# Optimization experiments

Hardware: AMD Instinct MI355X
Metric: run time of the kernel (lower is better)

The kernel has to match this reference:

```python
import jax, jax.numpy as jnp
import numpy as np

EPS = 1e-6
B, T, C = 2, 1024, 2048
H, KV, D = 32, 8, 128
E, F, TOPK = 8, 768, 2


def rmsnorm(x, w):
    xf = x.astype(jnp.float32)
    var = jnp.mean(xf * xf, axis=-1, keepdims=True)
    return w * (xf * jax.lax.rsqrt(var + EPS)).astype(x.dtype)


def rotate_half(x):
    d = x.shape[-1] // 2
    return jnp.concatenate([-x[..., d:], x[..., :d]], axis=-1)


def setup_inputs() -> dict:
    key = jax.random.key(0)
    ks = jax.random.split(key, 12)
    sc = 0.02
    x = jax.random.normal(ks[0], (B, T, C), dtype=jnp.float32)
    # RoPE tables: cos/sin of shape [B, T, D]
    inv_freq = 1.0 / (1e6 ** (np.arange(0, D, 2, dtype=np.float32) / D))
    pos = np.arange(T, dtype=np.float32)
    freqs = pos[:, None] * inv_freq[None, :]          # [T, D/2]
    emb = np.concatenate([freqs, freqs], axis=-1)     # [T, D]
    cos = jnp.broadcast_to(jnp.cos(emb)[None], (B, T, D)).astype(jnp.float32)
    sin = jnp.broadcast_to(jnp.sin(emb)[None], (B, T, D)).astype(jnp.float32)
    return {
        "x": x, "cos": cos, "sin": sin,
        "ln1_w": jnp.ones((C,), jnp.float32),
        "q_w": jax.random.normal(ks[1], (C, H * D), jnp.float32) * sc,
        "k_w": jax.random.normal(ks[2], (C, KV * D), jnp.float32) * sc,
        "v_w": jax.random.normal(ks[3], (C, KV * D), jnp.float32) * sc,
        "o_w": jax.random.normal(ks[4], (H * D, C), jnp.float32) * sc,
        "qn_w": jnp.ones((D,), jnp.float32),
        "kn_w": jnp.ones((D,), jnp.float32),
        "ln2_w": jnp.ones((C,), jnp.float32),
        "gate_w": jax.random.normal(ks[5], (C, E), jnp.float32) * sc,
        "gate_up_w": jax.random.normal(ks[6], (E, C, 2 * F), jnp.float32) * sc,
        "down_w": jax.random.normal(ks[7], (E, F, C), jnp.float32) * sc,
    }


def reference(x, cos, sin, ln1_w, q_w, k_w, v_w, o_w, qn_w, kn_w, ln2_w,
              gate_w, gate_up_w, down_w):
    b, t, c = x.shape
    # ---- attention branch ----
    h = rmsnorm(x, ln1_w)
    q = (h @ q_w).reshape(b, t, H, D)
    k = (h @ k_w).reshape(b, t, KV, D)
    v = (h @ v_w).reshape(b, t, KV, D)
    q = rmsnorm(q, qn_w)
    k = rmsnorm(k, kn_w)
    cb = cos[:, :, None, :]
    sb = sin[:, :, None, :]
    q = q * cb + rotate_half(q) * sb
    k = k * cb + rotate_half(k) * sb
    rep = H // KV
    k = jnp.repeat(k, rep, axis=2)  # [b,t,H,D]
    v = jnp.repeat(v, rep, axis=2)
    scores = jnp.einsum('bthd,bshd->bhts', q, k) / jnp.sqrt(jnp.float32(D))
    causal = jnp.tril(jnp.ones((t, t), dtype=bool))
    scores = jnp.where(causal, scores, jnp.finfo(scores.dtype).min)
    attn = jax.nn.softmax(scores, axis=-1)
    ao = jnp.einsum('bhts,bshd->bthd', attn, v).reshape(b, t, H * D) @ o_w
    x = x + ao
    # ---- MoE branch ----
    h2 = rmsnorm(x, ln2_w)
    hidden = h2.reshape(-1, c)                     # [N, C]
    logits = hidden @ gate_w                       # [N, E]
    rw = jax.nn.softmax(logits.astype(jnp.float32), axis=-1)
    tw, ti = jax.lax.top_k(rw, TOPK)
    tw = tw / (tw.sum(axis=-1, keepdims=True) + 1e-9)
    n = hidden.shape[0]
    routed = jnp.zeros_like(logits).at[jnp.arange(n)[:, None], ti].set(tw.astype(logits.dtype))
    routed = routed / (routed.sum(axis=-1, keepdims=True) + 1e-9)
    gu = jnp.einsum('th,ehq->teq', hidden, gate_up_w)   # [N, E, 2F]
    g, u = jnp.split(gu, 2, axis=-1)
    eo = jnp.einsum('teq,eqh->teh', jax.nn.silu(g) * u, down_w)  # [N, E, C]
    moe = (eo * routed[..., None]).sum(axis=1).reshape(b, t, c)
    return x + moe
```

## Files before the change

### kernel.cpp

```cpp
#include <hip/hip_runtime.h>
#include <hip/hip_bf16.h>

typedef short bf16x8 __attribute__((ext_vector_type(8)));
typedef float f32x4 __attribute__((ext_vector_type(4)));
typedef unsigned short u16;

#define NTOK 2048
#define CDIM 2048
#define TSEQ 1024
#define NH   32
#define NKV  8
#define DH   128
#define NE   8
#define FDIM 768
#define CAP  2048

#define GLOAD_LDS16(g, l) \
  __builtin_amdgcn_global_load_lds((const __attribute__((address_space(1))) void*)(g), \
                                   (__attribute__((address_space(3))) void*)(l), 16, 0, 0)

__device__ __forceinline__ u16 f2bf(float f){
  union { float f; unsigned u; } v; v.f = f;
  unsigned r = v.u + 0x7FFFu + ((v.u >> 16) & 1u);
  return (u16)(r >> 16);
}
__device__ __forceinline__ float bf2f(u16 x){
  union { unsigned u; float f; } v; v.u = ((unsigned)x) << 16; return v.f;
}

__device__ __forceinline__ f32x4 mfma_bf16(bf16x8 a, bf16x8 b, f32x4 c){
  return __builtin_amdgcn_mfma_f32_16x16x32_bf16(a, b, c, 0, 0, 0);
}

__device__ __forceinline__ int xcd_swz(int orig, int nwg){
  int xcd = orig & 7;
  int q = nwg >> 3, r = nwg & 7;
  int base = (xcd < r) ? xcd*(q+1) : r*(q+1) + (xcd-r)*q;
  return base + (orig >> 3);
}

__global__ void cast_transpose(const float* __restrict__ in, u16* __restrict__ out,
                               int R, int Cc, int rstride, int d1,
                               long long s_hi, long long s_lo)
{
  __shared__ u16 tile[64][72];
  int z = blockIdx.z;
  in  += (long long)(z / d1) * s_hi + (long long)(z % d1) * s_lo;
  out += (size_t)z * R * Cc;
  int r0 = blockIdx.y*64, c0 = blockIdx.x*64;
  int lr = threadIdx.x >> 4;
  int lc = (threadIdx.x & 15) * 4;
  #pragma unroll
  for(int i=0;i<4;i++){
    int r = lr + i*16;
    float4 v = *(const float4*)(in + (size_t)(r0 + r)*rstride + c0 + lc);
    tile[lc+0][r] = f2bf(v.x);
    tile[lc+1][r] = f2bf(v.y);
    tile[lc+2][r] = f2bf(v.z);
    tile[lc+3][r] = f2bf(v.w);
  }
  __syncthreads();
  int oc  = threadIdx.x >> 2;
  int orr = (threadIdx.x & 3) * 16;
  uint4 a  = *(const uint4*)&tile[oc][orr];
  uint4 b2 = *(const uint4*)&tile[oc][orr + 8];
  *(uint4*)(out + (size_t)(c0+oc)*R + r0 + orr)     = a;
  *(uint4*)(out + (size_t)(c0+oc)*R + r0 + orr + 8) = b2;
}

__global__ void cast_transpose_qkv(const float* __restrict__ qw, const float* __restrict__ kw,
                                   const float* __restrict__ vw, u16* __restrict__ wqkvT)
{
  __shared__ u16 tile[64][72];
  int bx = blockIdx.x;
  const float* in; u16* out; int rstride, c0;
  if(bx < 64){       in = qw; out = wqkvT;                        rstride = 4096; c0 = bx*64; }
  else if(bx < 80){  in = kw; out = wqkvT + (size_t)4096*2048;    rstride = 1024; c0 = (bx-64)*64; }
  else {             in = vw; out = wqkvT + (size_t)5120*2048;    rstride = 1024; c0 = (bx-80)*64; }
  const int R = 2048;
  int r0 = blockIdx.y*64;
  int lr = threadIdx.x >> 4;
  int lc = (threadIdx.x & 15) * 4;
  #pragma unroll
  for(int i=0;i<4;i++){
    int r = lr + i*16;
    float4 v = *(const float4*)(in + (size_t)(r0 + r)*rstride + c0 + lc);
    tile[lc+0][r] = f2bf(v.x);
    tile[lc+1][r] = f2bf(v.y);
    tile[lc+2][r] = f2bf(v.z);
    tile[lc+3][r] = f2bf(v.w);
  }
  __syncthreads();
  int oc  = threadIdx.x >> 2;
  int orr = (threadIdx.x & 3) * 16;
  uint4 a  = *(const uint4*)&tile[oc][orr];
  uint4 b2 = *(const uint4*)&tile[oc][orr + 8];
  *(uint4*)(out + (size_t)(c0+oc)*R + r0 + orr)     = a;
  *(uint4*)(out + (size_t)(c0+oc)*R + r0 + orr + 8) = b2;
}

__global__ void transpose_gate(const float* __restrict__ gw, float* __restrict__ gwT)
{
  int i = blockIdx.x*256 + threadIdx.x;
  int c = i >> 3, e = i & 7;
  gwT[(size_t)e*CDIM + c] = gw[(size_t)c*NE + e];
}

__global__ void transpose_u16(const u16* __restrict__ in, u16* __restrict__ out,
                              int R, int Cc, int rstride, int d1,
                              long long s_hi, long long s_lo)
{
  __shared__ u16 tile[32][34];
  int z = blockIdx.z;
  in += (long long)(z / d1) * s_hi + (long long)(z % d1) * s_lo;
  out += (size_t)z * R * Cc;
  int tx = threadIdx.x & 31, ty = threadIdx.x >> 5;
  int r0 = blockIdx.y * 32, c0 = blockIdx.x * 32;
  #pragma unroll
  for(int i=0;i<4;i++){
    int r = r0 + ty + i*8;
    if(r < R && c0 + tx < Cc) tile[ty + i*8][tx] = in[(size_t)r * rstride + c0 + tx];
  }
  __syncthreads();
  #pragma unroll
  for(int i=0;i<4;i++){
    int c = c0 + ty + i*8;
    if(c < Cc && r0 + tx < R) out[(size_t)c * R + r0 + tx] = tile[tx][ty + i*8];
  }
}

__global__ void rmsnorm_kernel(const float* __restrict__ x, const float* __restrict__ w,
                               u16* __restrict__ outb, float* __restrict__ outf)
{
  __shared__ float sbuf[4];
  int row = blockIdx.x;
  const float* xr = x + (size_t)row * CDIM;
  int t0 = threadIdx.x * 8;
  float4 v0 = *(const float4*)(xr + t0);
  float4 v1 = *(const float4*)(xr + t0 + 4);
  float a[8] = {v0.x,v0.y,v0.z,v0.w,v1.x,v1.y,v1.z,v1.w};
  float ss = 0.f;
  #pragma unroll
  for(int i=0;i<8;i++) ss += a[i]*a[i];
  #pragma unroll
  for(int o=32;o>0;o>>=1) ss += __shfl_xor(ss, o);
  if((threadIdx.x & 63) == 0) sbuf[threadIdx.x >> 6] = ss;
  __syncthreads();
  float tot = sbuf[0]+sbuf[1]+sbuf[2]+sbuf[3];
  float r = rsqrtf(tot * (1.0f/CDIM) + 1e-6f);
  float4 w0 = *(const float4*)(w + t0);
  float4 w1 = *(const float4*)(w + t0 + 4);
  float wv[8] = {w0.x,w0.y,w0.z,w0.w,w1.x,w1.y,w1.z,w1.w};
  #pragma unroll
  for(int i=0;i<8;i++){
    float o = a[i] * r * wv[i];
    outb[(size_t)row*CDIM + t0 + i] = f2bf(o);
    if(outf) outf[(size_t)row*CDIM + t0 + i] = o;
  }
}

__global__ __launch_bounds__(512, 1) void gemm256(const u16* __restrict__ A,
                                                  const u16* __restrict__ Bt,
                                                  u16* __restrict__ Cb,
                                                  int M, int N, int K)
{
  extern __shared__ u16 lds[];
  const int NT = K >> 6;
  int tid = threadIdx.x;
  int lane = tid & 63, g = lane >> 4, cl = lane & 15;
  int wid = tid >> 6, wr = wid >> 2, wc = wid & 3;
  int br = blockIdx.y * 256, bc = blockIdx.x * 192;
  int rowl[4], slotl[4], srcoff[4];
  #pragma unroll
  for(int l=0;l<4;l++){
    int c = l*512 + tid;
    rowl[l]  = c >> 3;
    slotl[l] = c & 7;
    srcoff[l] = (slotl[l] ^ (rowl[l] & 7)) * 8;
  }
  f32x4 acc[8][3];
  #pragma unroll
  for(int m=0;m<8;m++)
    #pragma unroll
    for(int n=0;n<3;n++) acc[m][n] = (f32x4){0.f,0.f,0.f,0.f};

  auto stage = [&](int t, int b){
    int k0 = t << 6;
    #pragma unroll
    for(int l=0;l<4;l++)
      GLOAD_LDS16(A  + (size_t)(br + rowl[l])*K + k0 + srcoff[l],
                  &lds[b*16384 + rowl[l]*64 + slotl[l]*8]);
    #pragma unroll
    for(int l=0;l<3;l++)
      GLOAD_LDS16(Bt + (size_t)(bc + rowl[l])*K + k0 + srcoff[l],
                  &lds[32768 + b*12288 + rowl[l]*64 + slotl[l]*8]);
  };

  stage(0, 0);
  for(int t=0;t<NT;t++){
    int buf = t & 1;
    if(t+1 < NT){
      stage(t+1, buf^1);
      asm volatile("s_waitcnt vmcnt(7)" ::: "memory");
    } else {
      asm volatile("s_waitcnt vmcnt(0)" ::: "memory");
    }
    asm volatile("s_barrier" ::: "memory");
    const u16* As_ = &lds[buf*16384];
    const u16* Bs_ = &lds[32768 + buf*12288];
    __builtin_amdgcn_s_setprio(1);
    #pragma unroll
    for(int kk=0;kk<2;kk++){
      bf16x8 a[8], b[3];
      #pragma unroll
      for(int m=0;m<8;m++){
        int row = wr*128 + m*16 + cl;
        int sl  = ((4*kk + g) ^ (row & 7)) * 8;
        a[m] = *(const bf16x8*)&As_[row*64 + sl];
      }
      #pragma unroll
      for(int n=0;n<3;n++){
        int row = wc*48 + n*16 + cl;
        int sl  = ((4*kk + g) ^ (row & 7)) * 8;
        b[n] = *(const bf16x8*)&Bs_[row*64 + sl];
      }
      #pragma unroll
      for(int m=0;m<8;m++)
        #pragma unroll
        for(int n=0;n<3;n++)
          acc[m][n] = mfma_bf16(a[m], b[n], acc[m][n]);
    }
    __builtin_amdgcn_s_setprio(0);
    asm volatile("s_barrier" ::: "memory");
  }
  #pragma unroll
  for(int m=0;m<8;m++)
    #pragma unroll
    for(int n=0;n<3;n++)
      #pragma unroll
      for(int j=0;j<4;j++){
        int row = br + wr*128 + m*16 + g*4 + j;
        int col = bc + wc*48 + n*16 + cl;
        Cb[(size_t)row*N + col] = f2bf(acc[m][n][j]);
      }
}

__global__ __launch_bounds__(256) void gemm_oproj_pipe(const u16* __restrict__ A,
                                                       const u16* __restrict__ Bt,
                                                       float* __restrict__ C,
                                                       const float* __restrict__ addsrc,
                                                       int M, int N, int K)
{
  extern __shared__ u16 lds[];
  int nwg = gridDim.x;
  int wgid = xcd_swz(blockIdx.x, nwg);
  int nbx = N >> 7;
  int bys = wgid / nbx, bxs = wgid % nbx;
  const int NT = K >> 6;
  int tid = threadIdx.x;
  int lane = tid&63, g = lane>>4, cl = lane&15;
  int w = tid>>6, wr = w>>1, wc = w&1;
  int br = bys*128, bc = bxs*128;
  int rowc[4], slotc[4], srcoff[4];
  #pragma unroll
  for(int l=0;l<4;l++){
    int c = l*256 + tid;
    rowc[l]  = c >> 3;
    slotc[l] = c & 7;
    srcoff[l] = (slotc[l] ^ (rowc[l] & 7)) * 8;
  }
  f32x4 acc[4][4];
  #pragma unroll
  for(int m=0;m<4;m++)
    #pragma unroll
    for(int n=0;n<4;n++) acc[m][n] = (f32x4){0.f,0.f,0.f,0.f};

  auto stage = [&](int t, int b){
    int k0 = t << 6;
    #pragma unroll
    for(int l=0;l<4;l++)
      GLOAD_LDS16(A + (size_t)(br + rowc[l])*K + k0 + srcoff[l],
                  &lds[b*8192 + rowc[l]*64 + slotc[l]*8]);
    #pragma unroll
    for(int l=0;l<4;l++)
      GLOAD_LDS16(Bt + (size_t)(bc + rowc[l])*K + k0 + srcoff[l],
                  &lds[16384 + b*8192 + rowc[l]*64 + slotc[l]*8]);
  };

  stage(0, 0);
  for(int t=0;t<NT;t++){
    int buf = t & 1;
    if(t+1 < NT){
      stage(t+1, buf^1);
      asm volatile("s_waitcnt vmcnt(8)" ::: "memory");
    } else {
      asm volatile("s_waitcnt vmcnt(0)" ::: "memory");
    }
    asm volatile("s_barrier" ::: "memory");
    const u16* As_ = &lds[buf*8192];
    const u16* Bs_ = &lds[16384 + buf*8192];
    __builtin_amdgcn_s_setprio(1);
    #pragma unroll
    for(int kk=0;kk<2;kk++){
      bf16x8 a[4], b[4];
      #pragma unroll
      for(int m=0;m<4;m++){
        int row = wr*64 + m*16 + cl;
        int sl  = ((4*kk + g) ^ (row & 7)) * 8;
        a[m] = *(const bf16x8*)&As_[row*64 + sl];
      }
      #pragma unroll
      for(int n=0;n<4;n++){
        int row = wc*64 + n*16 + cl;
        int sl  = ((4*kk + g) ^ (row & 7)) * 8;
        b[n] = *(const bf16x8*)&Bs_[row*64 + sl];
      }
      #pragma unroll
      for(int m=0;m<4;m++)
        #pragma unroll
        for(int n=0;n<4;n++)
          acc[m][n] = mfma_bf16(a[m], b[n], acc[m][n]);
    }
    __builtin_amdgcn_s_setprio(0);
    asm volatile("s_barrier" ::: "memory");
  }
  #pragma unroll
  for(int m=0;m<4;m++)
    #pragma unroll
    for(int n=0;n<4;n++)
      #pragma unroll
      for(int j=0;j<4;j++){
        int row = br + wr*64 + m*16 + g*4 + j;
        int col = bc + wc*64 + n*16 + cl;
        C[(size_t)row*N + col] = acc[m][n][j] + addsrc[(size_t)row*N + col];
      }
}

__global__ void qk_norm_rope(const u16* __restrict__ qkv, const float* __restrict__ cosb,
                             const float* __restrict__ sinb, const float* __restrict__ qnw,
                             const float* __restrict__ knw,
                             u16* __restrict__ qb, u16* __restrict__ kb)
{
  __shared__ float red[2];
  __shared__ float buf[128];
  int bt = blockIdx.x;
  int head = blockIdx.y;
  int d = threadIdx.x;
  int b = bt >> 10, t = bt & 1023;
  bool isq = head < NH;
  const u16* src = qkv + (size_t)bt*6144 + (isq ? head*DH : 4096 + (head-NH)*DH);
  float v = bf2f(src[d]);
  float ss = v*v;
  #pragma unroll
  for(int o=32;o>0;o>>=1) ss += __shfl_xor(ss, o);
  if((threadIdx.x & 63) == 0) red[threadIdx.x >> 6] = ss;
  __syncthreads();
  float tot = red[0] + red[1];
  float r = rsqrtf(tot * (1.0f/DH) + 1e-6f);
  float nv = v * r * (isq ? qnw[d] : knw[d]);
  buf[d] = nv;
  __syncthreads();
  float rot = (d < 64) ? -buf[d+64] : buf[d-64];
  float cs = cosb[(size_t)bt*DH + d], sn = sinb[(size_t)bt*DH + d];
  float ov = nv*cs + rot*sn;
  if(isq) ov *= 0.08838834764831845f;
  if(isq) qb[(((size_t)b*NH  + head)     *TSEQ + t)*DH + d] = f2bf(ov);
  else    kb[(((size_t)b*NKV + (head-NH))*TSEQ + t)*DH + d] = f2bf(ov);
}

__global__ __launch_bounds__(512) void attn_kernel(const u16* __restrict__ qb,
                                                   const u16* __restrict__ kb,
                                                   const u16* __restrict__ vt,
                                                   u16* __restrict__ aob)
{
  extern __shared__ u16 lds[];
  int tid = threadIdx.x;
  int w = tid>>6, lane = tid&63, g = lane>>4, cl = lane&15;
  int nwg = gridDim.x * gridDim.y * gridDim.z;
  int orig = (blockIdx.z * gridDim.y + blockIdx.y) * gridDim.x + blockIdx.x;
  int wgid = xcd_swz(orig, nwg);
  int bxs = wgid % gridDim.x;
  int bys = (wgid / gridDim.x) % gridDim.y;
  int bzs = wgid / (gridDim.x * gridDim.y);
  int b = bzs, kvh = bys, pr = bxs;
  int head = kvh*4 + (w>>1);
  int mh = w & 1;
  const u16* qp = qb + (((size_t)b*NH  + head)*TSEQ)*DH;
  const u16* kp = kb + (((size_t)b*NKV + kvh)*TSEQ)*DH;
  const u16* vp = vt + (((size_t)b*NKV + kvh)*DH)*TSEQ;
  u16* Psw = &lds[34816 + w*16*72];
  for(int idx = tid; idx < 2*16*64; idx += 512){
    int bufi = idx >> 10, rr = (idx >> 6) & 15, c2 = idx & 63;
    lds[16384 + bufi*9216 + (128 + rr)*64 + c2] = (rr == 0) ? (u16)0x3F80 : (u16)0;
  }
  __syncthreads();
  int kRow[2], kDst[2], kSrc[2], vRow[2], vDst[2], vSrc[2];
  #pragma unroll
  for(int it=0; it<2; it++){
    int c = tid + it*512;
    kRow[it] = c >> 4;
    int ks = c & 15;
    kDst[it] = kRow[it]*128 + ks*8;
    kSrc[it] = (ks ^ (kRow[it] & 7)) * 8;
    vRow[it] = c >> 3;
    int vs = c & 7;
    vDst[it] = vRow[it]*64 + vs*8;
    vSrc[it] = (vs ^ (vRow[it] & 7)) * 8;
  }
  int qts[2] = { pr, 31 - pr };
  for(int ti=0; ti<2; ti++){
    int qt = qts[ti];
    int q0 = qt*32;
    int qr0 = q0 + mh*16;
    const int NTk = (q0 + 95) >> 6;
    bf16x8 aq[4];
    #pragma unroll
    for(int kd=0;kd<4;kd++)
      aq[kd] = *(const bf16x8*)(qp + (size_t)(qr0 + cl)*DH + kd*32 + g*8);
    f32x4 accO[9];
    #pragma unroll
    for(int n=0;n<9;n++) accO[n] = (f32x4){0.f,0.f,0.f,0.f};
    float mr[4];
    #pragma unroll
    for(int j=0;j<4;j++) mr[j] = -1e30f;
    #pragma unroll
    for(int it=0; it<2; it++){
      GLOAD_LDS16(kp + (size_t)kRow[it]*DH + kSrc[it], &lds[kDst[it]]);
      GLOAD_LDS16(vp + (size_t)vRow[it]*TSEQ + vSrc[it], &lds[16384 + vDst[it]]);
    }
    for(int t=0; t<NTk; t++){
      int buf = t & 1;
      int kv0 = t*64;
      if(t+1 < NTk){
        int kv1 = kv0 + 64, nb = buf ^ 1;
        #pragma unroll
        for(int it=0; it<2; it++){
          GLOAD_LDS16(kp + (size_t)(kv1 + kRow[it])*DH + kSrc[it], &lds[nb*8192 + kDst[it]]);
          GLOAD_LDS16(vp + (size_t)vRow[it]*TSEQ + kv1 + vSrc[it], &lds[16384 + nb*9216 + vDst[it]]);
        }
        asm volatile("s_waitcnt vmcnt(4)" ::: "memory");
      } else {
        asm volatile("s_waitcnt vmcnt(0)" ::: "memory");
      }
      asm volatile("s_barrier" ::: "memory");
      const u16* Ksb = &lds[buf*8192];
      const u16* Vsb = &lds[16384 + buf*9216];
      f32x4 sc[4];
      #pragma unroll
      for(int n=0;n<4;n++) sc[n] = (f32x4){0.f,0.f,0.f,0.f};
      __builtin_amdgcn_s_setprio(1);
      #pragma unroll
      for(int kd=0;kd<4;kd++){
        bf16x8 bk[4];
        #pragma unroll
        for(int n=0;n<4;n++){
          int row = n*16 + cl;
          bk[n] = *(const bf16x8*)&Ksb[row*128 + (((kd*4 + g) ^ (cl & 7))*8)];
        }
        #pragma unroll
        for(int n=0;n<4;n++)
          sc[n] = mfma_bf16(aq[kd], bk[n], sc[n]);
      }
      __builtin_amdgcn_s_setprio(0);
      if(kv0 + 63 > q0){
        #pragma unroll
        for(int n=0;n<4;n++)
          #pragma unroll
          for(int j=0;j<4;j++){
            int row = qr0 + g*4 + j;
            int col = kv0 + n*16 + cl;
            if(col > row) sc[n][j] = -1e30f;
          }
      }
      float tmax[4];
      #pragma unroll
      for(int j=0;j<4;j++)
        tmax[j] = fmaxf(fmaxf(sc[0][j], sc[1][j]), fmaxf(sc[2][j], sc[3][j]));
      #pragma unroll
      for(int o=1;o<16;o<<=1)
        #pragma unroll
        for(int j=0;j<4;j++) tmax[j] = fmaxf(tmax[j], __shfl_xor(tmax[j], o));
      float grow = -1e30f;
      #pragma unroll
      for(int j=0;j<4;j++) grow = fmaxf(grow, tmax[j] - mr[j]);
      grow = fmaxf(grow, __shfl_xor(grow, 16));
      grow = fmaxf(grow, __shfl_xor(grow, 32));
      if(grow > 8.0f){
        #pragma unroll
        for(int j=0;j<4;j++){
          float mn = fmaxf(mr[j], tmax[j]);
          float f  = __expf(mr[j] - mn);
          mr[j] = mn;
          #pragma unroll
          for(int n=0;n<9;n++) accO[n][j] *= f;
        }
      }
      #pragma unroll
      for(int n=0;n<4;n++)
        #pragma unroll
        for(int j=0;j<4;j++)
          sc[n][j] = __expf(sc[n][j] - mr[j]);
      #pragma unroll
      for(int n=0;n<4;n++)
        #pragma unroll
        for(int j=0;j<4;j++)
          Psw[(g*4 + j)*72 + n*16 + cl] = f2bf(sc[n][j]);
      bf16x8 pa[2];
      #pragma unroll
      for(int s2=0;s2<2;s2++)
        pa[s2] = *(const bf16x8*)&Psw[cl*72 + s2*32 + g*8];
      __builtin_amdgcn_s_setprio(1);
      #pragma unroll
      for(int n=0;n<9;n++){
        #pragma unroll
        for(int s2=0;s2<2;s2++){
          bf16x8 bv = *(const bf16x8*)&Vsb[(n*16 + cl)*64 + (((s2*4 + g) ^ (cl & 7))*8)];
          accO[n] = mfma_bf16(pa[s2], bv, accO[n]);
        }
      }
      __builtin_amdgcn_s_setprio(0);
      asm volatile("s_barrier" ::: "memory");
    }
    float linv[4];
    #pragma unroll
    for(int j=0;j<4;j++){
      float l = __shfl(accO[8][j], lane & 48);
      linv[j] = 1.0f / l;
    }
    #pragma unroll
    for(int n=0;n<8;n++)
      #pragma unroll
      for(int j=0;j<4;j++){
        int row = qr0 + g*4 + j;
        float v = accO[n][j] * linv[j];
        aob[((size_t)b*TSEQ + row)*(NH*DH) + head*DH + n*16 + cl] = f2bf(v);
      }
  }
}

__global__ void route_kernel(const float* __restrict__ h2f, const float* __restrict__ gwT,
                             int* __restrict__ cnt, int* __restrict__ bidx,
                             float* __restrict__ bw)
{
  int lane = threadIdx.x & 63;
  int token = blockIdx.x*4 + (threadIdx.x >> 6);
  float acc[8];
  #pragma unroll
  for(int e=0;e<8;e++) acc[e]=0.f;
  for(int c0 = lane*4; c0 < CDIM; c0 += 256){
    float4 hv = *(const float4*)(h2f + (size_t)token*CDIM + c0);
    #pragma unroll
    for(int e=0;e<8;e++){
      float4 gv = *(const float4*)(gwT + (size_t)e*CDIM + c0);
      acc[e] += hv.x*gv.x + hv.y*gv.y + hv.z*gv.z + hv.w*gv.w;
    }
  }
  #pragma unroll
  for(int o=32;o>0;o>>=1)
    #pragma unroll
    for(int e=0;e<8;e++) acc[e] += __shfl_xor(acc[e], o);
  if(lane==0){
    float mx = acc[0];
    #pragma unroll
    for(int e=1;e<8;e++) mx = fmaxf(mx, acc[e]);
    float rw[8]; float s=0.f;
    #pragma unroll
    for(int e=0;e<8;e++){ rw[e] = __expf(acc[e]-mx); s += rw[e]; }
    #pragma unroll
    for(int e=0;e<8;e++) rw[e] /= s;
    int i0=0;
    #pragma unroll
    for(int e=1;e<8;e++) if(rw[e] > rw[i0]) i0=e;
    int i1 = (i0==0)?1:0;
    #pragma unroll
    for(int e=0;e<8;e++) if(e!=i0 && rw[e] > rw[i1]) i1=e;
    float tw0=rw[i0], tw1=rw[i1];
    float s1 = tw0+tw1+1e-9f;
    float a0 = tw0/s1, a1 = tw1/s1;
    float s2 = a0+a1+1e-9f;
    float w0 = a0/s2, w1 = a1/s2;
    int sl0 = atomicAdd(&cnt[i0],1);
    bidx[i0*CAP + sl0] = token; bw[i0*CAP + sl0] = w0;
    int sl1 = atomicAdd(&cnt[i1],1);
    bidx[i1*CAP + sl1] = token; bw[i1*CAP + sl1] = w1;
  }
}

__global__ __launch_bounds__(256) void gemm_gateup_pipe(const u16* __restrict__ h2b,
                                                        const u16* __restrict__ gupT,
                                                        u16* __restrict__ act,
                                                        const int* __restrict__ bidx,
                                                        const int* __restrict__ cnt)
{
  extern __shared__ u16 lds[];
  int d = blockIdx.x;
  int e = d & 7, j = d >> 3;
  int y = j / 12, x = j % 12;
  int nc = cnt[e];
  int sr = y*128;
  if(sr >= nc) return;
  const int K = CDIM, NT = K >> 6;
  const u16* Btg = gupT + (size_t)e*1536*CDIM + (size_t)(x*64)*CDIM;
  const u16* Btu = Btg + (size_t)768*CDIM;
  const int* be = bidx + e*CAP;
  int tid = threadIdx.x;
  int lane = tid&63, g = lane>>4, cl = lane&15;
  int w = tid>>6, wr = w>>1, wc = w&1;
  int rowA[4], slotA[4], srcA[4];
  long long atok[4];
  #pragma unroll
  for(int l=0;l<4;l++){
    int c = l*256 + tid;
    rowA[l]  = c >> 3;
    slotA[l] = c & 7;
    srcA[l] = (slotA[l] ^ (rowA[l] & 7)) * 8;
    int t = be[sr + rowA[l]];
    if(t < 0 || t >= NTOK) t = 0;
    atok[l] = (long long)t * CDIM;
  }
  int rowB[2], slotB[2], srcB[2];
  #pragma unroll
  for(int l=0;l<2;l++){
    int c = l*256 + tid;
    rowB[l]  = c >> 3;
    slotB[l] = c & 7;
    srcB[l] = (slotB[l] ^ (rowB[l] & 7)) * 8;
  }
  f32x4 accG[4][2], accU[4][2];
  #pragma unroll
  for(int m=0;m<4;m++)
    #pragma unroll
    for(int n=0;n<2;n++){ accG[m][n] = (f32x4){0.f,0.f,0.f,0.f}; accU[m][n] = (f32x4){0.f,0.f,0.f,0.f}; }

  auto stage = [&](int t, int b){
    int k0 = t << 6;
    #pragma unroll
    for(int l=0;l<4;l++)
      GLOAD_LDS16(h2b + atok[l] + k0 + srcA[l],
                  &lds[b*8192 + rowA[l]*64 + slotA[l]*8]);
    #pragma unroll
    for(int l=0;l<2;l++)
      GLOAD_LDS16(Btg + (size_t)rowB[l]*K + k0 + srcB[l],
                  &lds[16384 + b*4096 + rowB[l]*64 + slotB[l]*8]);
    #pragma unroll
    for(int l=0;l<2;l++)
      GLOAD_LDS16(Btu + (size_t)rowB[l]*K + k0 + srcB[l],
                  &lds[24576 + b*4096 + rowB[l]*64 + slotB[l]*8]);
  };

  stage(0, 0);
  for(int t=0;t<NT;t++){
    int buf = t & 1;
    if(t+1 < NT){
      stage(t+1, buf^1);
      asm volatile("s_waitcnt vmcnt(8)" ::: "memory");
    } else {
      asm volatile("s_waitcnt vmcnt(0)" ::: "memory");
    }
    asm volatile("s_barrier" ::: "memory");
    const u16* As_ = &lds[buf*8192];
    const u16* Bg_ = &lds[16384 + buf*4096];
    const u16* Bu_ = &lds[24576 + buf*4096];
    __builtin_amdgcn_s_setprio(1);
    #pragma unroll
    for(int kk=0;kk<2;kk++){
      bf16x8 a[4], bg[2], bu[2];
      #pragma unroll
      for(int m=0;m<4;m++){
        int row = wr*64 + m*16 + cl;
        int sl  = ((4*kk + g) ^ (row & 7)) * 8;
        a[m] = *(const bf16x8*)&As_[row*64 + sl];
      }
      #pragma unroll
      for(int n=0;n<2;n++){
        int row = wc*32 + n*16 + cl;
        int sl  = ((4*kk + g) ^ (row & 7)) * 8;
        bg[n] = *(const bf16x8*)&Bg_[row*64 + sl];
        bu[n] = *(const bf16x8*)&Bu_[row*64 + sl];
      }
      #pragma unroll
      for(int m=0;m<4;m++)
        #pragma unroll
        for(int n=0;n<2;n++){
          accG[m][n] = mfma_bf16(a[m], bg[n], accG[m][n]);
          accU[m][n] = mfma_bf16(a[m], bu[n], accU[m][n]);
        }
    }
    __builtin_amdgcn_s_setprio(0);
    asm volatile("s_barrier" ::: "memory");
  }
  #pragma unroll
  for(int m=0;m<4;m++)
    #pragma unroll
    for(int n=0;n<2;n++)
      #pragma unroll
      for(int jj=0;jj<4;jj++){
        int slot = sr + wr*64 + m*16 + g*4 + jj;
        int col  = x*64 + wc*32 + n*16 + cl;
        float gv = accG[m][n][jj], uv = accU[m][n][jj];
        float av = gv / (1.f + __expf(-gv)) * uv;
        act[((size_t)e*CAP + slot)*FDIM + col] = f2bf(av);
      }
}

__global__ __launch_bounds__(256) void gemm_down_pipe(const u16* __restrict__ act,
                                                      const u16* __restrict__ downT,
                                                      float* __restrict__ out,
                                                      const int* __restrict__ bidx,
                                                      const float* __restrict__ bw,
                                                      const int* __restrict__ cnt)
{
  extern __shared__ u16 lds[];
  int d = blockIdx.x;
  int e = d & 7, j = d >> 3;
  int y = j >> 4, x = j & 15;
  int nc = cnt[e];
  int sr = y*128;
  if(sr >= nc) return;
  const int K = FDIM, NT = K >> 6;
  const u16* A  = act   + ((size_t)e*CAP + sr)*FDIM;
  const u16* Bt = downT + (size_t)e*CDIM*FDIM + (size_t)(x*128)*FDIM;
  const int* be = bidx + e*CAP;
  const float* bwe = bw + e*CAP;
  int tid = threadIdx.x;
  int lane = tid&63, g = lane>>4, cl = lane&15;
  int w = tid>>6, wr = w>>1, wc = w&1;
  int rowc[4], slotc[4], srcoff[4];
  #pragma unroll
  for(int l=0;l<4;l++){
    int c = l*256 + tid;
    rowc[l]  = c >> 3;
    slotc[l] = c & 7;
    srcoff[l] = (slotc[l] ^ (rowc[l] & 7)) * 8;
  }
  f32x4 acc[4][4];
  #pragma unroll
  for(int m=0;m<4;m++)
    #pragma unroll
    for(int n=0;n<4;n++) acc[m][n] = (f32x4){0.f,0.f,0.f,0.f};

  auto stage = [&](int t, int b){
    int k0 = t << 6;
    #pragma unroll
    for(int l=0;l<4;l++)
      GLOAD_LDS16(A + (size_t)rowc[l]*K + k0 + srcoff[l],
                  &lds[b*8192 + rowc[l]*64 + slotc[l]*8]);
    #pragma unroll
    for(int l=0;l<4;l++)
      GLOAD_LDS16(Bt + (size_t)rowc[l]*K + k0 + srcoff[l],
                  &lds[16384 + b*8192 + rowc[l]*64 + slotc[l]*8]);
  };

  stage(0, 0);
  for(int t=0;t<NT;t++){
    int buf = t & 1;
    if(t+1 < NT){
      stage(t+1, buf^1);
      asm volatile("s_waitcnt vmcnt(8)" ::: "memory");
    } else {
      asm volatile("s_waitcnt vmcnt(0)" ::: "memory");
    }
    asm volatile("s_barrier" ::: "memory");
    const u16* As_ = &lds[buf*8192];
    const u16* Bs_ = &lds[16384 + buf*8192];
    __builtin_amdgcn_s_setprio(1);
    #pragma unroll
    for(int kk=0;kk<2;kk++){
      bf16x8 a[4], b[4];
      #pragma unroll
      for(int m=0;m<4;m++){
        int row = wr*64 + m*16 + cl;
        int sl  = ((4*kk + g) ^ (row & 7)) * 8;
        a[m] = *(const bf16x8*)&As_[row*64 + sl];
      }
      #pragma unroll
      for(int n=0;n<4;n++){
        int row = wc*64 + n*16 + cl;
        int sl  = ((4*kk + g) ^ (row & 7)) * 8;
        b[n] = *(const bf16x8*)&Bs_[row*64 + sl];
      }
      #pragma unroll
      for(int m=0;m<4;m++)
        #pragma unroll
        for(int n=0;n<4;n++)
          acc[m][n] = mfma_bf16(a[m], b[n], acc[m][n]);
    }
    __builtin_amdgcn_s_setprio(0);
    asm volatile("s_barrier" ::: "memory");
  }
  #pragma unroll
  for(int m=0;m<4;m++)
    #pragma unroll
    for(int jj=0;jj<4;jj++){
      int slot = sr + wr*64 + m*16 + g*4 + jj;
      if(slot < nc){
        int tok = be[slot];
        float wgt = bwe[slot];
        #pragma unroll
        for(int n=0;n<4;n++){
          int col = x*128 + wc*64 + n*16 + cl;
          atomicAdd(out + (size_t)tok*CDIM + col, wgt * acc[m][n][jj]);
        }
      }
    }
}

extern "C" void kernel_launch(void* const* d_in, const int* in_sizes, int n_in,
                              void* d_out, int out_size, void* d_ws, size_t ws_size,
                              hipStream_t stream)
{
  const float* x     = (const float*)d_in[0];
  const float* cosb  = (const float*)d_in[1];
  const float* sinb  = (const float*)d_in[2];
  const float* ln1w  = (const float*)d_in[3];
  const float* qw    = (const float*)d_in[4];
  const float* kw    = (const float*)d_in[5];
  const float* vw    = (const float*)d_in[6];
  const float* ow    = (const float*)d_in[7];
  const float* qnw   = (const float*)d_in[8];
  const float* knw   = (const float*)d_in[9];
  const float* ln2w  = (const float*)d_in[10];
  const float* gatew = (const float*)d_in[11];
  const float* gupw  = (const float*)d_in[12];
  const float* downw = (const float*)d_in[13];
  float* out = (float*)d_out;

  char* ws = (char*)d_ws;
  size_t off = 0;
  auto alloc = [&](size_t bytes)->char*{
    char* p = ws + off;
    off = (off + bytes + 255) & ~(size_t)255;
    return p;
  };
  u16*   wqkvT = (u16*)  alloc((size_t)6144*2048*2);
  u16*   owT   = (u16*)  alloc((size_t)2048*4096*2);
  u16*   gupT  = (u16*)  alloc((size_t)8*1536*2048*2);
  u16*   downT = (u16*)  alloc((size_t)8*2048*768*2);
  u16*   h1b   = (u16*)  alloc((size_t)2048*2048*2);
  u16*   qkvb  = (u16*)  alloc((size_t)2048*6144*2);
  u16*   qb    = (u16*)  alloc((size_t)2*32*1024*128*2);
  u16*   kb    = (u16*)  alloc((size_t)2*8*1024*128*2);
  u16*   vt    = (u16*)  alloc((size_t)2*8*1024*128*2);
  u16*   aob   = (u16*)  alloc((size_t)2048*4096*2);
  float* h2f   = (float*)alloc((size_t)2048*2048*4);
  u16*   h2b   = (u16*)  alloc((size_t)2048*2048*2);
  u16*   actb  = (u16*)  alloc((size_t)8*2048*768*2);
  int*   bidx  = (int*)  alloc((size_t)8*2048*4);
  float* bwgt  = (float*)alloc((size_t)8*2048*4);
  float* gwT   = (float*)alloc((size_t)8*2048*4);
  int*   cnt   = (int*)  alloc(64);
  (void)ws_size; (void)in_sizes; (void)n_in; (void)out_size;

  hipMemsetAsync(cnt, 0, 8*sizeof(int), stream);

  cast_transpose_qkv<<<dim3(96,32), 256, 0, stream>>>(qw, kw, vw, wqkvT);
  cast_transpose<<<dim3(32,64,1), 256, 0, stream>>>(ow, owT,      4096, 2048, 2048, 1, 0, 0);
  cast_transpose<<<dim3(24,32,8), 256, 0, stream>>>(gupw, gupT,   2048, 1536, 1536, 8, 0, (long long)2048*1536);
  cast_transpose<<<dim3(32,12,8), 256, 0, stream>>>(downw, downT, 768,  2048, 2048, 8, 0, (long long)768*2048);
  transpose_gate<<<64, 256, 0, stream>>>(gatew, gwT);

  rmsnorm_kernel<<<2048, 256, 0, stream>>>(x, ln1w, h1b, nullptr);
  gemm256<<<dim3(32,8), 512, 114688, stream>>>(h1b, wqkvT, qkvb, 2048, 6144, 2048);
  qk_norm_rope<<<dim3(2048,40), 128, 0, stream>>>(qkvb, cosb, sinb, qnw, knw, qb, kb);
  transpose_u16<<<dim3(4,32,16), 256, 0, stream>>>(qkvb + 5120, vt, 1024, 128, 6144, 8,
                                                   (long long)1024*6144, 128);
  attn_kernel<<<dim3(16,8,2), 512, 88064, stream>>>(qb, kb, vt, aob);
  gemm_oproj_pipe<<<256, 256, 65536, stream>>>(aob, owT, out, x, 2048, 2048, 4096);
  rmsnorm_kernel<<<2048, 256, 0, stream>>>(out, ln2w, h2b, h2f);
  route_kernel<<<512, 256, 0, stream>>>(h2f, gwT, cnt, bidx, bwgt);
  gemm_gateup_pipe<<<1536, 256, 65536, stream>>>(h2b, gupT, actb, bidx, cnt);
  gemm_down_pipe<<<2048, 256, 65536, stream>>>(actb, downT, out, bidx, bwgt, cnt);
}
```

Baseline: 432.5 us.

## Retile QKV GEMM to 256x256 with interleaved prefetch and XCD swizzle

The QKV projection GEMM now uses 256x256 output tiles instead of 256x192, launched as a 1D grid of 192 workgroups with XCD-aware swizzling. The K-loop is split into four phases, each loading a slice of A fragments and issuing part of the next tile's global-to-LDS loads before its MFMAs, so memory traffic overlaps compute rather than being issued all at once. B fragments are held in registers across phases. This raises LDS use to 128KB and accumulator register pressure, and adds more barriers per iteration. Fewer workgroups (192 versus 256) may leave some CUs idle.

```diff
diff --git a/kernel.cpp b/kernel.cpp
--- a/kernel.cpp
+++ b/kernel.cpp
@@ -169,80 +169,147 @@
   int tid = threadIdx.x;
   int lane = tid & 63, g = lane >> 4, cl = lane & 15;
   int wid = tid >> 6, wr = wid >> 2, wc = wid & 3;
-  int br = blockIdx.y * 256, bc = blockIdx.x * 192;
-  int rowl[4], slotl[4], srcoff[4];
+  int nwg = gridDim.x;
+  int wgid = xcd_swz(blockIdx.x, nwg);
+  int nbx = N >> 8;
+  int bys = wgid / nbx, bxs = wgid % nbx;
+  int br = bys*256, bc = bxs*256;
+  int rowl[4], slotl[4], srcoff[4], dstl[4];
   #pragma unroll
   for(int l=0;l<4;l++){
     int c = l*512 + tid;
     rowl[l]  = c >> 3;
     slotl[l] = c & 7;
     srcoff[l] = (slotl[l] ^ (rowl[l] & 7)) * 8;
-  }
-  f32x4 acc[8][3];
+    dstl[l]  = rowl[l]*64 + slotl[l]*8;
+  }
+  f32x4 acc[8][4];
   #pragma unroll
   for(int m=0;m<8;m++)
     #pragma unroll
-    for(int n=0;n<3;n++) acc[m][n] = (f32x4){0.f,0.f,0.f,0.f};
-
-  auto stage = [&](int t, int b){
-    int k0 = t << 6;
-    #pragma unroll
-    for(int l=0;l<4;l++)
-      GLOAD_LDS16(A  + (size_t)(br + rowl[l])*K + k0 + srcoff[l],
-                  &lds[b*16384 + rowl[l]*64 + slotl[l]*8]);
-    #pragma unroll
-    for(int l=0;l<3;l++)
-      GLOAD_LDS16(Bt + (size_t)(bc + rowl[l])*K + k0 + srcoff[l],
-                  &lds[32768 + b*12288 + rowl[l]*64 + slotl[l]*8]);
-  };
-
-  stage(0, 0);
-  for(int t=0;t<NT;t++){
-    int buf = t & 1;
-    if(t+1 < NT){
-      stage(t+1, buf^1);
-      asm volatile("s_waitcnt vmcnt(7)" ::: "memory");
-    } else {
-      asm volatile("s_waitcnt vmcnt(0)" ::: "memory");
-    }
+    for(int n=0;n<4;n++) acc[m][n] = (f32x4){0.f,0.f,0.f,0.f};
+
+#define GA_(l, t, b) GLOAD_LDS16(A  + (size_t)(br + rowl[l])*K + ((t)<<6) + srcoff[l], \
+                                 &lds[(b)*16384 + dstl[l]])
+#define GB_(l, t, b) GLOAD_LDS16(Bt + (size_t)(bc + rowl[l])*K + ((t)<<6) + srcoff[l], \
+                                 &lds[32768 + (b)*16384 + dstl[l]])
+#define CFENCE asm volatile("" ::: "memory")
+
+  GB_(0,0,0); GB_(1,0,0); CFENCE;
+  GB_(2,0,0); GB_(3,0,0); CFENCE;
+  GA_(0,0,0); GA_(2,0,0); CFENCE;
+  GA_(1,0,0); GA_(3,0,0); CFENCE;
+
+  for(int t=0; t<NT; t++){
+    int buf = t & 1, nb = buf ^ 1;
+    bool pf = (t+1 < NT);
+    const u16* As_ = &lds[buf*16384];
+    const u16* Bs_ = &lds[32768 + buf*16384];
+    bf16x8 bfr[4][2], afr[2][2];
+
+    if(pf) asm volatile("s_waitcnt vmcnt(2)" ::: "memory");
+    else   asm volatile("s_waitcnt vmcnt(0)" ::: "memory");
     asm volatile("s_barrier" ::: "memory");
-    const u16* As_ = &lds[buf*16384];
-    const u16* Bs_ = &lds[32768 + buf*12288];
+    #pragma unroll
+    for(int n=0;n<4;n++)
+      #pragma unroll
+      for(int kk=0;kk<2;kk++){
+        int row = wc*64 + n*16 + cl;
+        bfr[n][kk] = *(const bf16x8*)&Bs_[row*64 + (((4*kk + g) ^ (row & 7))*8)];
+      }
+    #pragma unroll
+    for(int i=0;i<2;i++)
+      #pragma unroll
+      for(int kk=0;kk<2;kk++){
+        int row = wr*128 + i*16 + cl;
+        afr[i][kk] = *(const bf16x8*)&As_[row*64 + (((4*kk + g) ^ (row & 7))*8)];
+      }
+    if(pf){ GB_(0,t+1,nb); GB_(1,t+1,nb); }
+    CFENCE;
     __builtin_amdgcn_s_setprio(1);
     #pragma unroll
-    for(int kk=0;kk<2;kk++){
-      bf16x8 a[8], b[3];
-      #pragma unroll
-      for(int m=0;m<8;m++){
-        int row = wr*128 + m*16 + cl;
-        int sl  = ((4*kk + g) ^ (row & 7)) * 8;
-        a[m] = *(const bf16x8*)&As_[row*64 + sl];
-      }
-      #pragma unroll
-      for(int n=0;n<3;n++){
-        int row = wc*48 + n*16 + cl;
-        int sl  = ((4*kk + g) ^ (row & 7)) * 8;
-        b[n] = *(const bf16x8*)&Bs_[row*64 + sl];
-      }
-      #pragma unroll
-      for(int m=0;m<8;m++)
-        #pragma unroll
-        for(int n=0;n<3;n++)
-          acc[m][n] = mfma_bf16(a[m], b[n], acc[m][n]);
-    }
+    for(int kk=0;kk<2;kk++)
+      #pragma unroll
+      for(int i=0;i<2;i++)
+        #pragma unroll
+        for(int n=0;n<4;n++)
+          acc[i][n] = mfma_bf16(afr[i][kk], bfr[n][kk], acc[i][n]);
     __builtin_amdgcn_s_setprio(0);
+
     asm volatile("s_barrier" ::: "memory");
+    #pragma unroll
+    for(int i=0;i<2;i++)
+      #pragma unroll
+      for(int kk=0;kk<2;kk++){
+        int row = wr*128 + (2+i)*16 + cl;
+        afr[i][kk] = *(const bf16x8*)&As_[row*64 + (((4*kk + g) ^ (row & 7))*8)];
+      }
+    if(pf){ GB_(2,t+1,nb); GB_(3,t+1,nb); }
+    CFENCE;
+    __builtin_amdgcn_s_setprio(1);
+    #pragma unroll
+    for(int kk=0;kk<2;kk++)
+      #pragma unroll
+      for(int i=0;i<2;i++)
+        #pragma unroll
+        for(int n=0;n<4;n++)
+          acc[2+i][n] = mfma_bf16(afr[i][kk], bfr[n][kk], acc[2+i][n]);
+    __builtin_amdgcn_s_setprio(0);
+
+    if(pf) asm volatile("s_waitcnt vmcnt(4)" ::: "memory");
+    asm volatile("s_barrier" ::: "memory");
+    #pragma unroll
+    for(int i=0;i<2;i++)
+      #pragma unroll
+      for(int kk=0;kk<2;kk++){
+        int row = wr*128 + (4+i)*16 + cl;
+        afr[i][kk] = *(const bf16x8*)&As_[row*64 + (((4*kk + g) ^ (row & 7))*8)];
+      }
+    if(pf){ GA_(0,t+1,nb); GA_(2,t+1,nb); }
+    CFENCE;
+    __builtin_amdgcn_s_setprio(1);
+    #pragma unroll
+    for(int kk=0;kk<2;kk++)
+      #pragma unroll
+      for(int i=0;i<2;i++)
+        #pragma unroll
+        for(int n=0;n<4;n++)
+          acc[4+i][n] = mfma_bf16(afr[i][kk], bfr[n][kk], acc[4+i][n]);
+    __builtin_amdgcn_s_setprio(0);
+
+    asm volatile("s_barrier" ::: "memory");
+    #pragma unroll
+    for(int i=0;i<2;i++)
+      #pragma unroll
+      for(int kk=0;kk<2;kk++){
+        int row = wr*128 + (6+i)*16 + cl;
+        afr[i][kk] = *(const bf16x8*)&As_[row*64 + (((4*kk + g) ^ (row & 7))*8)];
+      }
+    if(pf){ GA_(1,t+1,nb); GA_(3,t+1,nb); }
+    CFENCE;
+    __builtin_amdgcn_s_setprio(1);
+    #pragma unroll
+    for(int kk=0;kk<2;kk++)
+      #pragma unroll
+      for(int i=0;i<2;i++)
+        #pragma unroll
+        for(int n=0;n<4;n++)
+          acc[6+i][n] = mfma_bf16(afr[i][kk], bfr[n][kk], acc[6+i][n]);
+    __builtin_amdgcn_s_setprio(0);
   }
   #pragma unroll
   for(int m=0;m<8;m++)
     #pragma unroll
-    for(int n=0;n<3;n++)
+    for(int n=0;n<4;n++)
       #pragma unroll
       for(int j=0;j<4;j++){
         int row = br + wr*128 + m*16 + g*4 + j;
-        int col = bc + wc*48 + n*16 + cl;
+        int col = bc + wc*64 + n*16 + cl;
         Cb[(size_t)row*N + col] = f2bf(acc[m][n][j]);
       }
+#undef GA_
+#undef GB_
+#undef CFENCE
 }
 
 __global__ __launch_bounds__(256) void gemm_oproj_pipe(const u16* __restrict__ A,
@@ -860,7 +927,7 @@
   transpose_gate<<<64, 256, 0, stream>>>(gatew, gwT);
 
   rmsnorm_kernel<<<2048, 256, 0, stream>>>(x, ln1w, h1b, nullptr);
-  gemm256<<<dim3(32,8), 512, 114688, stream>>>(h1b, wqkvT, qkvb, 2048, 6144, 2048);
+  gemm256<<<192, 512, 131072, stream>>>(h1b, wqkvT, qkvb, 2048, 6144, 2048);
   qk_norm_rope<<<dim3(2048,40), 128, 0, stream>>>(qkvb, cosb, sinb, qnw, knw, qb, kb);
   transpose_u16<<<dim3(4,32,16), 256, 0, stream>>>(qkvb + 5120, vt, 1024, 128, 6144, 8,
                                                    (long long)1024*6144, 128);
```

New measurement: 435.5 us. Within noise of the previous version (+0.7%).
